# Kernel optimization log

Measured on AMD Instinct MI355X. Metric: run time of the kernel, lower is better.

The kernel has to match this reference:

```python
import jax, jax.numpy as jnp
import numpy as np

B, S, N, F, H = 128, 128, 24, 16, 32  # batch, seq, nodes, in-feat/node, hid/node


def setup_inputs() -> dict:
    key = jax.random.key(0)
    ks = jax.random.split(key, 7)
    IS, HS = N * F, N * H
    stdv = 1.0 / np.sqrt(HS).astype(np.float32)
    x = jax.random.normal(ks[0], (B, S, N, F), jnp.float32)
    h0 = jax.random.normal(ks[1], (B, N, H), jnp.float32)
    c0 = jax.random.normal(ks[2], (B, N, H), jnp.float32)
    G = jax.random.normal(ks[3], (N, N), jnp.float32)
    W = jax.random.uniform(ks[4], (IS, 4 * HS), jnp.float32, -stdv, stdv)
    U = jax.random.uniform(ks[5], (HS, 4 * HS), jnp.float32, -stdv, stdv)
    bias = jax.random.uniform(ks[6], (4 * HS,), jnp.float32, -stdv, stdv)
    return {"x": x, "h0": h0, "c0": c0, "W": W, "U": U, "bias": bias, "G": G}


def _graph_masks(G, F, H):
    # repeat_interleave(G, r, dim=-2) == kron(G, ones(r,1)); dim=-1 == kron(G, ones(1,c)).
    # Then tile x4 along last dim for the 4 LSTM gates.
    GW = jnp.tile(jnp.kron(G, jnp.ones((F, H), G.dtype)), (1, 4))  # [N*F, 4*N*H]
    GU = jnp.tile(jnp.kron(G, jnp.ones((H, H), G.dtype)), (1, 4))  # [N*H, 4*N*H]
    return GW, GU


def reference(x, h0, c0, W, U, bias, G):
    B, S, N, F = x.shape
    H = h0.shape[-1]
    HS = N * H
    GW, GU = _graph_masks(G, F, H)
    Wm = W * GW                      # masked input weights
    Um = U * GU                      # masked recurrent weights
    # Non-recurrent term batched into one big GEMM over all timesteps.
    xf = x.reshape(B, S, N * F)
    xg = jnp.einsum('bsi,ig->bsg', xf, Wm) + bias  # [B,S,4*HS]
    h = h0.reshape(B, HS)
    c = c0.reshape(B, HS)

    def step(carry, xg_t):
        h, c = carry
        gates = xg_t + h @ Um
        i = jax.nn.sigmoid(gates[:, :HS])
        f = jax.nn.sigmoid(gates[:, HS:2 * HS])
        g = jnp.tanh(gates[:, 2 * HS:3 * HS])
        o = jax.nn.sigmoid(gates[:, 3 * HS:])
        c = f * c + i * g
        h = o * jnp.tanh(c)
        return (h, c), h

    (h, c), hs = jax.lax.scan(step, (h, c), jnp.swapaxes(xg, 0, 1))  # hs: [S,B,HS]
    hidden_seq = jnp.swapaxes(hs, 0, 1).reshape(B, S, N, H)
    return hidden_seq, (h.reshape(B, N, H), c.reshape(B, N, H))
```

## Files before the change

kernel.cpp:

```cpp
#include <hip/hip_runtime.h>
#include <hip/hip_bf16.h>


typedef __bf16 bf16x8 __attribute__((ext_vector_type(8)));
typedef float f32x4 __attribute__((ext_vector_type(4)));

#define HS 768
#define GATES 3072
#define KV 1152
#define SEQ 128
#define BATCH 128
#define OUT_HID (BATCH*SEQ*HS)
#define BPITCH 1160
#define NWG 192
#define TEAM_WGS 24

__device__ __forceinline__ float fast_sig(float x) {
    return 1.0f / (1.0f + __expf(-x));
}
__device__ __forceinline__ float fast_tanh(float x) {
    x = fminf(fmaxf(x, -15.0f), 15.0f);
    float e = __expf(2.0f * x);
    return (e - 1.0f) / (e + 1.0f);
}

__device__ __forceinline__ bf16x8 cvt8(const float* src) {
    float4 v0 = *(const float4*)src;
    float4 v1 = *(const float4*)(src + 4);
    bf16x8 p;
    p[0] = (__bf16)v0.x; p[1] = (__bf16)v0.y; p[2] = (__bf16)v0.z; p[3] = (__bf16)v0.w;
    p[4] = (__bf16)v1.x; p[5] = (__bf16)v1.y; p[6] = (__bf16)v1.z; p[7] = (__bf16)v1.w;
    return p;
}

__device__ __forceinline__ int swz(int c8, int row) {
    return (c8 & ~3) | ((c8 & 3) ^ (row & 3));
}

__global__ void prep_kernel(const float* __restrict__ W, const float* __restrict__ U,
                            const float* __restrict__ G, __bf16* __restrict__ VmT) {
    __shared__ __bf16 tile[64][65];
    const int kvb = blockIdx.x * 64;
    const int cb  = blockIdx.y * 64;
    const int tid = threadIdx.x;
    {
        const int cl = tid & 63, kl0 = tid >> 6;
        #pragma unroll
        for (int i = 0; i < 16; ++i) {
            int kl = kl0 + i * 4;
            int kv = kvb + kl;
            int c  = cb + cl;
            int nout = (c % HS) >> 5;
            float g, v;
            if (kv < 384) {
                g = G[(kv >> 4) * 24 + nout];
                v = W[(size_t)kv * GATES + c];
            } else {
                int ku = kv - 384;
                g = G[(ku >> 5) * 24 + nout];
                v = U[(size_t)ku * GATES + c];
            }
            tile[kl][cl] = (__bf16)(v * g);
        }
    }
    __syncthreads();
    {
        const int kl = tid & 63, cl0 = tid >> 6;
        #pragma unroll
        for (int i = 0; i < 16; ++i) {
            int c = cl0 + i * 4;
            VmT[(size_t)(cb + c) * KV + kvb + kl] = tile[kl][c];
        }
    }
}

__global__ void prep_x(const float* __restrict__ x, __bf16* __restrict__ xb) {
    const int g = blockIdx.x * 256 + threadIdx.x;
    const int e = g * 8;
    const int b = e / (SEQ * 384);
    const int rem = e - b * (SEQ * 384);
    const int t = rem / 384;
    const int k = rem - t * 384;
    *(bf16x8*)&xb[((size_t)t * BATCH + b) * 384 + k] = cvt8(&x[e]);
}

__global__ __launch_bounds__(256, 1) void scan_kernel(
        const __bf16* __restrict__ xb,
        const float* __restrict__ h0,
        const float* __restrict__ c0,
        const __bf16* __restrict__ VmT,
        const float* __restrict__ bias,
        float* out,
        unsigned* xh32,
        unsigned* bar) {
    __shared__ __align__(16) __bf16 Bs[16 * BPITCH];
    const int tid = threadIdx.x;
    const int lane = tid & 63, wv = tid >> 6;
    const int m = lane & 15, quad = lane >> 4;
    const int team = blockIdx.x & 7, wg = blockIdx.x >> 3;
    const int bbase = team * 16;
    const int jbase = wg * 32 + wv * 8;

    unsigned* flags = bar;
    unsigned* myflag = flags + (team * TEAM_WGS + wg) * 16;

    bf16x8 w[2][36];
    #pragma unroll
    for (int T = 0; T < 2; ++T) {
        const int cg = (m & 3) * HS + jbase + 2 * (m >> 2) + T;
        const __bf16* wp = VmT + (size_t)cg * KV;
        #pragma unroll
        for (int kk = 0; kk < 36; ++kk)
            w[T][kk] = *(const bf16x8*)(wp + kk * 32 + quad * 8);
    }

    const int b_own = bbase + m;
    const int j0 = jbase + 2 * quad;
    const int j1 = j0 + 1;
    float cv0 = c0[b_own * HS + j0];
    float cv1 = c0[b_own * HS + j1];
    f32x4 bias0, bias1;
    #pragma unroll
    for (int r = 0; r < 4; ++r) {
        bias0[r] = bias[r * HS + j0];
        bias1[r] = bias[r * HS + j1];
    }

    const int bq = (quad ^ (m & 3));

    #pragma unroll
    for (int i = 0; i < 3; ++i) {
        int ch = tid + i * 256;
        int row = ch / 48, c8 = ch % 48;
        *(uint4*)&Bs[row * BPITCH + swz(c8, row) * 8] =
            *(const uint4*)&xb[((size_t)0 * BATCH + bbase + row) * 384 + c8 * 8];
    }
    #pragma unroll
    for (int i = 0; i < 6; ++i) {
        int ch = tid + i * 256;
        int row = ch / 96, c8h = ch % 96;
        bf16x8 p = cvt8(&h0[(size_t)(bbase + row) * HS + c8h * 8]);
        *(bf16x8*)&Bs[row * BPITCH + (48 + swz(c8h, row)) * 8] = p;
    }
    __syncthreads();

    #pragma unroll 1
    for (int t = 0; t < SEQ; ++t) {
        f32x4 acc0 = bias0, acc1 = bias1;
        #pragma unroll
        for (int kk = 0; kk < 36; ++kk) {
            bf16x8 bf = *(const bf16x8*)&Bs[m * BPITCH + kk * 32 + bq * 8];
            acc0 = __builtin_amdgcn_mfma_f32_16x16x32_bf16(w[0][kk], bf, acc0, 0, 0, 0);
            acc1 = __builtin_amdgcn_mfma_f32_16x16x32_bf16(w[1][kk], bf, acc1, 0, 0, 0);
        }

        float h0v, h1v;
        {
            float ii = fast_sig(acc0[0]), ff = fast_sig(acc0[1]);
            float gg = fast_tanh(acc0[2]), oo = fast_sig(acc0[3]);
            cv0 = ff * cv0 + ii * gg;
            h0v = oo * fast_tanh(cv0);
        }
        {
            float ii = fast_sig(acc1[0]), ff = fast_sig(acc1[1]);
            float gg = fast_tanh(acc1[2]), oo = fast_sig(acc1[3]);
            cv1 = ff * cv1 + ii * gg;
            h1v = oo * fast_tanh(cv1);
        }

        if (t == SEQ - 1) {
            const size_t obase = ((size_t)b_own * SEQ + t) * HS;
            out[obase + j0] = h0v;
            out[obase + j1] = h1v;
            out[OUT_HID + b_own * HS + j0] = h0v;
            out[OUT_HID + b_own * HS + j1] = h1v;
            out[OUT_HID + BATCH * HS + b_own * HS + j0] = cv0;
            out[OUT_HID + BATCH * HS + b_own * HS + j1] = cv1;
            break;
        }

        {
            unsigned lo = (unsigned)__builtin_bit_cast(unsigned short, (__bf16)h0v);
            unsigned hi = (unsigned)__builtin_bit_cast(unsigned short, (__bf16)h1v);
            unsigned* dst = xh32 + ((size_t)(t & 1) * BATCH + b_own) * 384
                                 + (jbase >> 1) + quad;
            __hip_atomic_store(dst, lo | (hi << 16), __ATOMIC_RELAXED,
                               __HIP_MEMORY_SCOPE_AGENT);
        }
        {
            const size_t obase = ((size_t)b_own * SEQ + t) * HS;
            out[obase + j0] = h0v;
            out[obase + j1] = h1v;
        }

        __syncthreads();

        if (tid == 0)
            __hip_atomic_store(myflag, (unsigned)(t + 1), __ATOMIC_RELAXED,
                               __HIP_MEMORY_SCOPE_AGENT);

        #pragma unroll
        for (int i = 0; i < 3; ++i) {
            int ch = tid + i * 256;
            int row = ch / 48, c8 = ch % 48;
            *(uint4*)&Bs[row * BPITCH + swz(c8, row) * 8] =
                *(const uint4*)&xb[((size_t)(t + 1) * BATCH + bbase + row) * 384 + c8 * 8];
        }

        if (wv == 0 && lane < TEAM_WGS) {
            const unsigned* fp = flags + (team * TEAM_WGS + lane) * 16;
            while (__hip_atomic_load(fp, __ATOMIC_RELAXED,
                                     __HIP_MEMORY_SCOPE_AGENT) < (unsigned)(t + 1)) {
            }
        }
        __syncthreads();

        {
            const unsigned* src = xh32 + (size_t)(t & 1) * BATCH * 384;
            unsigned vals[24];
            #pragma unroll
            for (int i = 0; i < 24; ++i) {
                int ch = tid + i * 256;
                int row = ch / 384, u = ch % 384;
                vals[i] = __hip_atomic_load(&src[(size_t)(bbase + row) * 384 + u],
                                            __ATOMIC_RELAXED, __HIP_MEMORY_SCOPE_AGENT);
            }
            #pragma unroll
            for (int i = 0; i < 24; ++i) {
                int ch = tid + i * 256;
                int row = ch / 384, u = ch % 384;
                int c8h = u >> 2;
                int eo = (u & 3) * 2;
                *(unsigned*)&Bs[row * BPITCH + (48 + swz(c8h, row)) * 8 + eo] = vals[i];
            }
        }
        __syncthreads();
    }
}

extern "C" void kernel_launch(void* const* d_in, const int* in_sizes, int n_in,
                              void* d_out, int out_size, void* d_ws, size_t ws_size,
                              hipStream_t stream) {
    (void)in_sizes; (void)n_in; (void)out_size; (void)ws_size;
    const float* x    = (const float*)d_in[0];
    const float* h0   = (const float*)d_in[1];
    const float* c0   = (const float*)d_in[2];
    const float* W    = (const float*)d_in[3];
    const float* U    = (const float*)d_in[4];
    const float* bias = (const float*)d_in[5];
    const float* G    = (const float*)d_in[6];
    float* out = (float*)d_out;

    char* wsb = (char*)d_ws;
    unsigned* bar = (unsigned*)wsb;
    __bf16* VmT  = (__bf16*)(wsb + 16384);
    __bf16* xb   = (__bf16*)(wsb + 16384 + (size_t)GATES * KV * 2);
    unsigned* xh32 = (unsigned*)(wsb + 16384 + (size_t)GATES * KV * 2
                                      + (size_t)SEQ * BATCH * 384 * 2);

    hipMemsetAsync(bar, 0, 16384, stream);
    prep_kernel<<<dim3(18, 48), 256, 0, stream>>>(W, U, G, VmT);
    prep_x<<<dim3(3072), 256, 0, stream>>>(x, xb);
    scan_kernel<<<dim3(NWG), dim3(256), 0, stream>>>(xb, h0, c0, VmT, bias,
                                                     out, xh32, bar);
}
```

Baseline: 591.2 us.

## Compute input-projection MFMAs for next step before waiting on team barrier

Moves the x-part of the gate GEMM (first 12 k-blocks) out of the per-step LDS loop. It is now computed straight from global memory into a separate accumulator right after publishing h, so it overlaps the inter-workgroup flag wait. LDS now holds only h, with a new pitch and no swizzle, and h is gathered with 64-bit atomic loads. The barrier before the gather is dropped because every wave now spins on the flags itself. Output stores become float2. In exchange, every wave polls the flags, and the unswizzled LDS layout may cause bank conflicts.

New measurement: 745.2 us. 1.26x slower.

```diff
diff --git a/kernel.cpp b/kernel.cpp
--- a/kernel.cpp
+++ b/kernel.cpp
@@ -11,7 +11,7 @@
 #define SEQ 128
 #define BATCH 128
 #define OUT_HID (BATCH*SEQ*HS)
-#define BPITCH 1160
+#define LPITCH 1584
 #define NWG 192
 #define TEAM_WGS 24
 
@@ -31,10 +31,6 @@
     p[0] = (__bf16)v0.x; p[1] = (__bf16)v0.y; p[2] = (__bf16)v0.z; p[3] = (__bf16)v0.w;
     p[4] = (__bf16)v1.x; p[5] = (__bf16)v1.y; p[6] = (__bf16)v1.z; p[7] = (__bf16)v1.w;
     return p;
-}
-
-__device__ __forceinline__ int swz(int c8, int row) {
-    return (c8 & ~3) | ((c8 & 3) ^ (row & 3));
 }
 
 __global__ void prep_kernel(const float* __restrict__ W, const float* __restrict__ U,
@@ -93,7 +89,7 @@
         float* out,
         unsigned* xh32,
         unsigned* bar) {
-    __shared__ __align__(16) __bf16 Bs[16 * BPITCH];
+    __shared__ __align__(16) char Bs[16 * LPITCH];
     const int tid = threadIdx.x;
     const int lane = tid & 63, wv = tid >> 6;
     const int m = lane & 15, quad = lane >> 4;
@@ -126,32 +122,35 @@
         bias1[r] = bias[r * HS + j1];
     }
 
-    const int bq = (quad ^ (m & 3));
-
-    #pragma unroll
-    for (int i = 0; i < 3; ++i) {
-        int ch = tid + i * 256;
-        int row = ch / 48, c8 = ch % 48;
-        *(uint4*)&Bs[row * BPITCH + swz(c8, row) * 8] =
-            *(const uint4*)&xb[((size_t)0 * BATCH + bbase + row) * 384 + c8 * 8];
-    }
     #pragma unroll
     for (int i = 0; i < 6; ++i) {
         int ch = tid + i * 256;
         int row = ch / 96, c8h = ch % 96;
         bf16x8 p = cvt8(&h0[(size_t)(bbase + row) * HS + c8h * 8]);
-        *(bf16x8*)&Bs[row * BPITCH + (48 + swz(c8h, row)) * 8] = p;
+        *(bf16x8*)(Bs + row * LPITCH + c8h * 16) = p;
     }
     __syncthreads();
+
+    f32x4 accA0 = bias0, accA1 = bias1;
+    {
+        const __bf16* xrow = xb + ((size_t)0 * BATCH + bbase + m) * 384 + quad * 8;
+        #pragma unroll
+        for (int kk = 0; kk < 12; ++kk) {
+            bf16x8 xf = *(const bf16x8*)(xrow + kk * 32);
+            accA0 = __builtin_amdgcn_mfma_f32_16x16x32_bf16(w[0][kk], xf, accA0, 0, 0, 0);
+            accA1 = __builtin_amdgcn_mfma_f32_16x16x32_bf16(w[1][kk], xf, accA1, 0, 0, 0);
+        }
+    }
 
     #pragma unroll 1
     for (int t = 0; t < SEQ; ++t) {
-        f32x4 acc0 = bias0, acc1 = bias1;
-        #pragma unroll
-        for (int kk = 0; kk < 36; ++kk) {
-            bf16x8 bf = *(const bf16x8*)&Bs[m * BPITCH + kk * 32 + bq * 8];
-            acc0 = __builtin_amdgcn_mfma_f32_16x16x32_bf16(w[0][kk], bf, acc0, 0, 0, 0);
-            acc1 = __builtin_amdgcn_mfma_f32_16x16x32_bf16(w[1][kk], bf, acc1, 0, 0, 0);
+        f32x4 acc0 = accA0, acc1 = accA1;
+        const char* hbase = Bs + m * LPITCH + quad * 16;
+        #pragma unroll
+        for (int p = 0; p < 24; ++p) {
+            bf16x8 bf = *(const bf16x8*)(hbase + p * 64);
+            acc0 = __builtin_amdgcn_mfma_f32_16x16x32_bf16(w[0][12 + p], bf, acc0, 0, 0, 0);
+            acc1 = __builtin_amdgcn_mfma_f32_16x16x32_bf16(w[1][12 + p], bf, acc1, 0, 0, 0);
         }
 
         float h0v, h1v;
@@ -170,12 +169,9 @@
 
         if (t == SEQ - 1) {
             const size_t obase = ((size_t)b_own * SEQ + t) * HS;
-            out[obase + j0] = h0v;
-            out[obase + j1] = h1v;
-            out[OUT_HID + b_own * HS + j0] = h0v;
-            out[OUT_HID + b_own * HS + j1] = h1v;
-            out[OUT_HID + BATCH * HS + b_own * HS + j0] = cv0;
-            out[OUT_HID + BATCH * HS + b_own * HS + j1] = cv1;
+            *(float2*)&out[obase + j0] = make_float2(h0v, h1v);
+            *(float2*)&out[OUT_HID + b_own * HS + j0] = make_float2(h0v, h1v);
+            *(float2*)&out[OUT_HID + BATCH * HS + b_own * HS + j0] = make_float2(cv0, cv1);
             break;
         }
 
@@ -189,8 +185,7 @@
         }
         {
             const size_t obase = ((size_t)b_own * SEQ + t) * HS;
-            out[obase + j0] = h0v;
-            out[obase + j1] = h1v;
+            *(float2*)&out[obase + j0] = make_float2(h0v, h1v);
         }
 
         __syncthreads();
@@ -199,39 +194,41 @@
             __hip_atomic_store(myflag, (unsigned)(t + 1), __ATOMIC_RELAXED,
                                __HIP_MEMORY_SCOPE_AGENT);
 
-        #pragma unroll
-        for (int i = 0; i < 3; ++i) {
-            int ch = tid + i * 256;
-            int row = ch / 48, c8 = ch % 48;
-            *(uint4*)&Bs[row * BPITCH + swz(c8, row) * 8] =
-                *(const uint4*)&xb[((size_t)(t + 1) * BATCH + bbase + row) * 384 + c8 * 8];
-        }
-
-        if (wv == 0 && lane < TEAM_WGS) {
+        accA0 = bias0; accA1 = bias1;
+        {
+            const __bf16* xrow = xb + ((size_t)(t + 1) * BATCH + bbase + m) * 384
+                               + quad * 8;
+            #pragma unroll
+            for (int kk = 0; kk < 12; ++kk) {
+                bf16x8 xf = *(const bf16x8*)(xrow + kk * 32);
+                accA0 = __builtin_amdgcn_mfma_f32_16x16x32_bf16(w[0][kk], xf, accA0, 0, 0, 0);
+                accA1 = __builtin_amdgcn_mfma_f32_16x16x32_bf16(w[1][kk], xf, accA1, 0, 0, 0);
+            }
+        }
+
+        if (lane < TEAM_WGS) {
             const unsigned* fp = flags + (team * TEAM_WGS + lane) * 16;
             while (__hip_atomic_load(fp, __ATOMIC_RELAXED,
                                      __HIP_MEMORY_SCOPE_AGENT) < (unsigned)(t + 1)) {
             }
         }
-        __syncthreads();
-
-        {
-            const unsigned* src = xh32 + (size_t)(t & 1) * BATCH * 384;
-            unsigned vals[24];
+
+        {
+            const unsigned long long* src64 =
+                (const unsigned long long*)xh32 + (size_t)(t & 1) * BATCH * 192;
+            unsigned long long v[12];
             #pragma unroll
-            for (int i = 0; i < 24; ++i) {
-                int ch = tid + i * 256;
-                int row = ch / 384, u = ch % 384;
-                vals[i] = __hip_atomic_load(&src[(size_t)(bbase + row) * 384 + u],
-                                            __ATOMIC_RELAXED, __HIP_MEMORY_SCOPE_AGENT);
+            for (int i = 0; i < 12; ++i) {
+                int g = tid + i * 256;
+                int row = g / 192, du = g % 192;
+                v[i] = __hip_atomic_load(&src64[(size_t)(bbase + row) * 192 + du],
+                                         __ATOMIC_RELAXED, __HIP_MEMORY_SCOPE_AGENT);
             }
             #pragma unroll
-            for (int i = 0; i < 24; ++i) {
-                int ch = tid + i * 256;
-                int row = ch / 384, u = ch % 384;
-                int c8h = u >> 2;
-                int eo = (u & 3) * 2;
-                *(unsigned*)&Bs[row * BPITCH + (48 + swz(c8h, row)) * 8 + eo] = vals[i];
+            for (int i = 0; i < 12; ++i) {
+                int g = tid + i * 256;
+                int row = g / 192, du = g % 192;
+                *(unsigned long long*)(Bs + row * LPITCH + du * 8) = v[i];
             }
         }
         __syncthreads();
```
